# Kernel tuning notes

Measured on AMD Instinct MI355X. Metric: run time of the kernel, lower is better.

## Reference

```python
import jax, jax.numpy as jnp
import numpy as np

N_NODES = 20000
N_EDGES = 320000
F_IN = 512
F_OUT = 1024
N_GRAPHS = 64


def gcn_conv(x, src, dst, ew, W, b, n_nodes):
    xw = x @ W  # [N, Fout]
    loop = jnp.arange(n_nodes)
    s = jnp.concatenate([src, loop])
    d = jnp.concatenate([dst, loop])
    w = jnp.concatenate([ew, jnp.ones((n_nodes,), dtype=x.dtype)])
    deg = jax.ops.segment_sum(w, d, num_segments=n_nodes)  # in-degree by weight
    dinv = jnp.where(deg > 0, jax.lax.rsqrt(deg), 0.0).astype(x.dtype)
    norm = dinv[s] * w * dinv[d]  # [E+N]
    msg = norm[:, None] * xw[s]  # [E+N, Fout]
    out = jax.ops.segment_sum(msg, d, num_segments=n_nodes)
    return out + b


def mean_pool(x, batch, n_graphs):
    sums = jax.ops.segment_sum(x, batch, num_segments=n_graphs)
    cnt = jax.ops.segment_sum(jnp.ones((x.shape[0],), dtype=x.dtype), batch, num_segments=n_graphs)
    return sums / jnp.maximum(cnt, 1.0)[:, None]


def setup_inputs() -> dict:
    key = jax.random.key(0)
    ks = jax.random.split(key, 8)
    node_features = jax.random.normal(ks[0], (N_NODES, F_IN), dtype=jnp.float32)
    edge_index = jax.random.randint(ks[1], (2, N_EDGES), 0, N_NODES, dtype=jnp.int64)
    edge_weight = jax.random.uniform(ks[2], (N_EDGES,), dtype=jnp.float32)
    batch = jnp.sort(jax.random.randint(ks[3], (N_NODES,), 0, N_GRAPHS, dtype=jnp.int64))
    # Glorot-style params for the two GCNConv layers
    W1 = jax.random.normal(ks[4], (F_IN, F_OUT), dtype=jnp.float32) / np.sqrt(F_IN)
    b1 = jnp.zeros((F_OUT,), dtype=jnp.float32)
    W2 = jax.random.normal(ks[5], (F_OUT, F_OUT), dtype=jnp.float32) / np.sqrt(F_OUT)
    b2 = jnp.zeros((F_OUT,), dtype=jnp.float32)
    return {"node_features": node_features, "edge_index": edge_index,
            "edge_weight": edge_weight, "batch": batch,
            "W1": W1, "b1": b1, "W2": W2, "b2": b2}


def reference(node_features, edge_index, edge_weight, batch, W1, b1, W2, b2):
    n_nodes = node_features.shape[0]
    src, dst = edge_index[0], edge_index[1]
    h = jax.nn.relu(gcn_conv(node_features, src, dst, edge_weight, W1, b1, n_nodes))
    h = jax.nn.relu(gcn_conv(h, src, dst, edge_weight, W2, b2, n_nodes))
    return mean_pool(h, batch, N_GRAPHS)  # [G, F_OUT]
```

## Files before the change

### kernel.cpp

```cpp
#include <hip/hip_runtime.h>

#define N_NODES 20000
#define N_PAD   20480
#define N_EDGES 320000
#define F_IN 512
#define F_OUT 1024
#define N_GRAPHS 64
#define ESTRIDE 64

typedef __attribute__((ext_vector_type(8))) short bf16x8;
typedef __attribute__((ext_vector_type(4))) float f32x4;
typedef __attribute__((ext_vector_type(8))) unsigned short ushort8v;

static __device__ __forceinline__ unsigned short f2bf(float f) {
    unsigned int u = __float_as_uint(f);
    u = (u + 0x7fff + ((u >> 16) & 1)) >> 16;
    return (unsigned short)u;
}
static __device__ __forceinline__ float bf2f(unsigned short s) {
    return __uint_as_float(((unsigned int)s) << 16);
}

__global__ void k_setup(float* deg, int* cursor, float* out,
                        const int* __restrict__ batch, int* gstart,
                        unsigned int* __restrict__ csre) {
    int i = blockIdx.x * 256 + threadIdx.x;
    if (i < N_NODES) { deg[i] = 1.0f; cursor[i] = 0; }
    if (i < N_GRAPHS * F_OUT) out[i] = 0.f;
    if (i <= N_GRAPHS) {
        if (i == N_GRAPHS) gstart[i] = N_NODES;
        else {
            int lo = 0, hi = N_NODES;
            while (lo < hi) {
                int mid = (lo + hi) >> 1;
                if (batch[mid] < i) lo = mid + 1; else hi = mid;
            }
            gstart[i] = lo;
        }
    }
    for (int t = i; t < N_NODES * ESTRIDE; t += 65536) csre[t] = 0u;
}

#define NB_E    ((N_EDGES + 255) / 256)
#define NB_WT   ((F_OUT / 32) * (F_IN / 32 + F_OUT / 32))
#define NB_CX   (N_PAD * (F_IN / 8) / 256)
__global__ __launch_bounds__(256) void k_pre(const int* __restrict__ dst,
                                             const float* __restrict__ ew,
                                             float* deg,
                                             const float* __restrict__ W1,
                                             unsigned short* __restrict__ Wt1,
                                             const float* __restrict__ W2,
                                             unsigned short* __restrict__ Wt2,
                                             const float* __restrict__ x,
                                             unsigned short* __restrict__ xb) {
    __shared__ float tile[32][33];
    const int bid = blockIdx.x;
    if (bid < NB_E) {
        int e = bid * 256 + threadIdx.x;
        if (e < N_EDGES) atomicAdd(&deg[dst[e]], ew[e]);
    } else if (bid < NB_E + NB_WT) {
        int cid = bid - NB_E;
        int by = cid >> 5;
        int n0 = (cid & 31) * 32;
        const float* W; unsigned short* Wt; int K, k0;
        if (by < F_IN / 32) { W = W1; Wt = Wt1; K = F_IN;  k0 = by * 32; }
        else                { W = W2; Wt = Wt2; K = F_OUT; k0 = (by - F_IN / 32) * 32; }
        int tx = threadIdx.x & 31;
        int ty = threadIdx.x >> 5;
#pragma unroll
        for (int i = 0; i < 32; i += 8)
            tile[ty + i][tx] = W[(size_t)(k0 + ty + i) * F_OUT + n0 + tx];
        __syncthreads();
#pragma unroll
        for (int i = 0; i < 32; i += 8)
            Wt[(size_t)(n0 + ty + i) * K + k0 + tx] = f2bf(tile[tx][ty + i]);
    } else {
        int idx = (bid - NB_E - NB_WT) * 256 + threadIdx.x;
        int row = idx >> 6;
        int c8 = (idx & 63) * 8;
        if (row >= N_PAD) return;
        ushort8v v;
        if (row < N_NODES) {
            const float* p = &x[(size_t)row * F_IN + c8];
#pragma unroll
            for (int i = 0; i < 8; i++) v[i] = f2bf(p[i]);
        } else {
#pragma unroll
            for (int i = 0; i < 8; i++) v[i] = 0;
        }
        *(ushort8v*)&xb[(size_t)row * F_IN + c8] = v;
    }
}

__global__ void k_fill(const int* __restrict__ src, const int* __restrict__ dst,
                       const float* __restrict__ ew, const float* __restrict__ deg,
                       int* cursor, unsigned int* __restrict__ csre) {
    int e = blockIdx.x * 256 + threadIdx.x;
    if (e < N_EDGES) {
        int d = dst[e], s = src[e];
        int pos = atomicAdd(&cursor[d], 1);
        if (pos < ESTRIDE) {
            float w = rsqrtf(deg[s]) * ew[e] * rsqrtf(deg[d]);
            csre[d * ESTRIDE + pos] = ((unsigned int)f2bf(w) << 16) | (unsigned int)s;
        }
    }
}

__global__ __launch_bounds__(256) void k_aggr_slab(const unsigned short* __restrict__ xin,
                                                   const float* __restrict__ deg,
                                                   const int* __restrict__ cursor,
                                                   const unsigned int* __restrict__ csre,
                                                   const float* __restrict__ bias,
                                                   unsigned short* __restrict__ outp,
                                                   int F, int act) {
    const int bid = blockIdx.x;
    const int slab = bid & 7;
    const int ng = (bid >> 3) * 4 + (threadIdx.x >> 6);
    const int lane = threadIdx.x & 63;
    const int n = ng * 8 + (lane >> 3);
    const int c = blockIdx.y * 512 + slab * 64 + (lane & 7) * 8;

    if (n >= N_NODES) {
        ushort8v z;
#pragma unroll
        for (int i = 0; i < 8; i++) z[i] = 0;
        *(ushort8v*)&outp[(size_t)n * F + c] = z;
        return;
    }

    const float di = rsqrtf(deg[n]);
    const float wself = di * di;
    float a[8];
    {
        ushort8v v = *(const ushort8v*)&xin[(size_t)n * F + c];
#pragma unroll
        for (int i = 0; i < 8; i++) a[i] = bf2f(v[i]) * wself;
    }

    const unsigned int* ce = csre + (size_t)n * ESTRIDE;
    const int cnt = min(cursor[n], ESTRIDE);
    const int cnt4 = (cnt + 3) & ~3;

    if (cnt4 > 0) {
        uint4 m0 = *(const uint4*)&ce[0];
        uint4 m1 = (4 < cnt4) ? *(const uint4*)&ce[4] : m0;
        ushort8v u0 = *(const ushort8v*)&xin[(size_t)(m0.x & 0xFFFF) * F + c];
        ushort8v u1 = *(const ushort8v*)&xin[(size_t)(m0.y & 0xFFFF) * F + c];
        ushort8v u2 = *(const ushort8v*)&xin[(size_t)(m0.z & 0xFFFF) * F + c];
        ushort8v u3 = *(const ushort8v*)&xin[(size_t)(m0.w & 0xFFFF) * F + c];

        for (int j = 4; j < cnt4; j += 4) {
            ushort8v v0 = *(const ushort8v*)&xin[(size_t)(m1.x & 0xFFFF) * F + c];
            ushort8v v1 = *(const ushort8v*)&xin[(size_t)(m1.y & 0xFFFF) * F + c];
            ushort8v v2 = *(const ushort8v*)&xin[(size_t)(m1.z & 0xFFFF) * F + c];
            ushort8v v3 = *(const ushort8v*)&xin[(size_t)(m1.w & 0xFFFF) * F + c];
            const int jn = (j + 4 < cnt4) ? j + 4 : 0;
            uint4 m2 = *(const uint4*)&ce[jn];
            {
                float w0 = bf2f((unsigned short)(m0.x >> 16));
                float w1 = bf2f((unsigned short)(m0.y >> 16));
                float w2 = bf2f((unsigned short)(m0.z >> 16));
                float w3 = bf2f((unsigned short)(m0.w >> 16));
#pragma unroll
                for (int i = 0; i < 8; i++) {
                    a[i] += w0 * bf2f(u0[i]);
                    a[i] += w1 * bf2f(u1[i]);
                    a[i] += w2 * bf2f(u2[i]);
                    a[i] += w3 * bf2f(u3[i]);
                }
            }
            m0 = m1; m1 = m2;
            u0 = v0; u1 = v1; u2 = v2; u3 = v3;
        }
        {
            float w0 = bf2f((unsigned short)(m0.x >> 16));
            float w1 = bf2f((unsigned short)(m0.y >> 16));
            float w2 = bf2f((unsigned short)(m0.z >> 16));
            float w3 = bf2f((unsigned short)(m0.w >> 16));
#pragma unroll
            for (int i = 0; i < 8; i++) {
                a[i] += w0 * bf2f(u0[i]);
                a[i] += w1 * bf2f(u1[i]);
                a[i] += w2 * bf2f(u2[i]);
                a[i] += w3 * bf2f(u3[i]);
            }
        }
    }

    ushort8v r;
    if (act) {
#pragma unroll
        for (int i = 0; i < 8; i++) r[i] = f2bf(fmaxf(a[i] + bias[c + i], 0.f));
    } else {
#pragma unroll
        for (int i = 0; i < 8; i++) r[i] = f2bf(a[i]);
    }
    *(ushort8v*)&outp[(size_t)n * F + c] = r;
}

__global__ __launch_bounds__(256, 3) void k_gemm_sb(const unsigned short* __restrict__ A,
                                                    const unsigned short* __restrict__ Bt,
                                                    unsigned short* __restrict__ C, int K,
                                                    const float* __restrict__ bias, int act) {
    __shared__ short As[128 * 64];
    __shared__ short Bs[128 * 64];
    const int bid = blockIdx.x;
    const int xcd = bid & 7;
    const int i2 = bid >> 3;
    const int colb = i2 & 7;
    const int rowb = xcd * 20 + (i2 >> 3);
    const int row0 = rowb * 128;
    const int col0 = colb * 128;

    const int tid = threadIdx.x;
    const int lane = tid & 63;
    const int wave = tid >> 6;
    const int wm = wave >> 1, wn = wave & 1;
    const int l16 = lane & 15;
    const int kq = lane >> 4;

    const int NT = K >> 6;
    f32x4 acc[4][4] = {};

    for (int t = 0; t < NT; ++t) {
        const int k0 = t * 64;
#pragma unroll
        for (int it = 0; it < 4; it++) {
            int q = it * 256 + tid;
            int r = q >> 3;
            int g = (q & 7) ^ (r & 7);
            __builtin_amdgcn_global_load_lds(
                (const __attribute__((address_space(1))) void*)&A[(size_t)(row0 + r) * K + k0 + g * 8],
                (__attribute__((address_space(3))) void*)&As[q * 8], 16, 0, 0);
            __builtin_amdgcn_global_load_lds(
                (const __attribute__((address_space(1))) void*)&Bt[(size_t)(col0 + r) * K + k0 + g * 8],
                (__attribute__((address_space(3))) void*)&Bs[q * 8], 16, 0, 0);
        }
        __syncthreads();

#pragma unroll
        for (int ks = 0; ks < 2; ks++) {
            bf16x8 af[4], bfr[4];
#pragma unroll
            for (int fr = 0; fr < 4; fr++) {
                int r = wm * 64 + fr * 16 + l16;
                int g = (ks * 4 + kq) ^ (r & 7);
                af[fr] = *(const bf16x8*)&As[(r * 8 + g) * 8];
            }
#pragma unroll
            for (int fc = 0; fc < 4; fc++) {
                int r = wn * 64 + fc * 16 + l16;
                int g = (ks * 4 + kq) ^ (r & 7);
                bfr[fc] = *(const bf16x8*)&Bs[(r * 8 + g) * 8];
            }
            __builtin_amdgcn_s_setprio(1);
#pragma unroll
            for (int fr = 0; fr < 4; fr++)
#pragma unroll
                for (int fc = 0; fc < 4; fc++)
                    acc[fr][fc] = __builtin_amdgcn_mfma_f32_16x16x32_bf16(
                        af[fr], bfr[fc], acc[fr][fc], 0, 0, 0);
            __builtin_amdgcn_s_setprio(0);
        }
        __syncthreads();
    }

#pragma unroll
    for (int fr = 0; fr < 4; fr++) {
        int m0 = row0 + wm * 64 + fr * 16 + kq * 4;
#pragma unroll
        for (int fc = 0; fc < 4; fc++) {
            int n = col0 + wn * 64 + fc * 16 + l16;
            float bv = act ? bias[n] : 0.f;
#pragma unroll
            for (int reg = 0; reg < 4; reg++) {
                float v = acc[fr][fc][reg];
                if (act) v = fmaxf(v + bv, 0.f);
                C[(size_t)(m0 + reg) * F_OUT + n] = f2bf(v);
            }
        }
    }
}

__global__ __launch_bounds__(64) void k_pool_g(const unsigned short* __restrict__ h,
                                               const int* __restrict__ gstart,
                                               float* __restrict__ out) {
    const int g = blockIdx.x >> 4;
    const int slab = blockIdx.x & 15;
    const int lane = threadIdx.x;
    const int c = slab * 64 + (lane & 7) * 8;
    const int r0 = gstart[g], r1 = gstart[g + 1];

    float a[8] = {};
    for (int r = r0 + (lane >> 3); r < r1; r += 8) {
        ushort8v v = *(const ushort8v*)&h[(size_t)r * F_OUT + c];
#pragma unroll
        for (int i = 0; i < 8; i++) a[i] += bf2f(v[i]);
    }
#pragma unroll
    for (int m = 8; m < 64; m <<= 1)
#pragma unroll
        for (int i = 0; i < 8; i++) a[i] += __shfl_xor(a[i], m, 64);

    if ((lane >> 3) == 0) {
        const float inv = 1.0f / (float)max(r1 - r0, 1);
#pragma unroll
        for (int i = 0; i < 8; i++)
            out[(size_t)g * F_OUT + c + i] = a[i] * inv;
    }
}

extern "C" void kernel_launch(void* const* d_in, const int* in_sizes, int n_in,
                              void* d_out, int out_size, void* d_ws, size_t ws_size,
                              hipStream_t stream) {
    const float* x    = (const float*)d_in[0];
    const int* ei     = (const int*)d_in[1];
    const float* ew   = (const float*)d_in[2];
    const int* batch  = (const int*)d_in[3];
    const float* W1   = (const float*)d_in[4];
    const float* b1   = (const float*)d_in[5];
    const float* W2   = (const float*)d_in[6];
    const float* b2   = (const float*)d_in[7];
    float* out = (float*)d_out;

    const int* src = ei;
    const int* dst = ei + N_EDGES;

    char* ws = (char*)d_ws;
    const size_t SZ_XB  = (size_t)N_PAD * F_IN * 2;
    const size_t SZ_AX  = (size_t)N_PAD * F_IN * 2;
    const size_t SZ_WT1 = (size_t)F_OUT * F_IN * 2;
    const size_t SZ_WT2 = (size_t)F_OUT * F_OUT * 2;
    const size_t SZ_B   = (size_t)N_PAD * F_OUT * 2;
    unsigned short* xb  = (unsigned short*)(ws);
    unsigned short* ax  = (unsigned short*)(ws + SZ_XB);
    unsigned short* Wt1 = (unsigned short*)(ws + SZ_XB + SZ_AX);
    unsigned short* Wt2 = (unsigned short*)(ws + SZ_XB + SZ_AX + SZ_WT1);
    unsigned short* h1  = (unsigned short*)(ws + SZ_XB + SZ_AX + SZ_WT1 + SZ_WT2);
    unsigned short* xw2 = (unsigned short*)(ws + SZ_XB + SZ_AX + SZ_WT1 + SZ_WT2 + SZ_B);
    unsigned short* h2  = (unsigned short*)(ws);
    size_t off = SZ_XB + SZ_AX + SZ_WT1 + SZ_WT2 + 2 * SZ_B;
    auto alloc = [&](size_t bytes) -> void* {
        void* p = ws + off;
        off += (bytes + 255) & ~(size_t)255;
        return p;
    };
    float*        deg    = (float*)       alloc((size_t)N_NODES * 4);
    int*          cursor = (int*)         alloc((size_t)N_NODES * 4);
    unsigned int* csre   = (unsigned int*)alloc((size_t)N_NODES * ESTRIDE * 4);
    int*          gstart = (int*)         alloc((size_t)(N_GRAPHS + 1) * 4);

    k_setup<<<(N_GRAPHS * F_OUT + 255) / 256, 256, 0, stream>>>(deg, cursor, out, batch, gstart, csre);
    k_pre<<<NB_E + NB_WT + NB_CX, 256, 0, stream>>>(dst, ew, deg, W1, Wt1, W2, Wt2, x, xb);
    k_fill<<<NB_E, 256, 0, stream>>>(src, dst, ew, deg, cursor, csre);
    k_aggr_slab<<<dim3((N_PAD / 32) * 8, 1), 256, 0, stream>>>(xb, deg, cursor, csre,
                                                               (const float*)nullptr, ax, F_IN, 0);
    const int gemm_blocks = (N_PAD / 128) * (F_OUT / 128);
    k_gemm_sb<<<gemm_blocks, 256, 0, stream>>>(ax, Wt1, h1, F_IN, b1, 1);
    k_gemm_sb<<<gemm_blocks, 256, 0, stream>>>(h1, Wt2, xw2, F_OUT, (const float*)nullptr, 0);
    k_aggr_slab<<<dim3((N_PAD / 32) * 8, 2), 256, 0, stream>>>(xw2, deg, cursor, csre, b2, h2, F_OUT, 1);
    k_pool_g<<<N_GRAPHS * 16, 64, 0, stream>>>(h2, gstart, out);
}
```

Baseline: 313.6 us.

## Widen GEMM tile to 128x256 with 8 waves and cheapen gather address math

The GEMM kernel now uses 512-thread blocks computing 128x256 output tiles (8 waves in a 2x4 layout), halving the number of blocks and reusing each A tile across twice as many columns. In the aggregation kernel, gather addresses are computed with 32-bit shifts instead of 64-bit multiplies, and bf16 edge weights are extracted with a mask instead of shift-and-convert. The larger tile raises LDS use and register pressure per block, which may lower occupancy.

```diff
diff --git a/kernel.cpp b/kernel.cpp
--- a/kernel.cpp
+++ b/kernel.cpp
@@ -128,11 +128,15 @@
         return;
     }
 
+    const char* xb_ = (const char*)xin;
+    const unsigned shB = (F == 512) ? 10u : 11u;
+    const unsigned c2 = (unsigned)(c * 2);
+
     const float di = rsqrtf(deg[n]);
     const float wself = di * di;
     float a[8];
     {
-        ushort8v v = *(const ushort8v*)&xin[(size_t)n * F + c];
+        ushort8v v = *(const ushort8v*)(xb_ + (((unsigned)n << shB) + c2));
 #pragma unroll
         for (int i = 0; i < 8; i++) a[i] = bf2f(v[i]) * wself;
     }
@@ -144,23 +148,23 @@
     if (cnt4 > 0) {
         uint4 m0 = *(const uint4*)&ce[0];
         uint4 m1 = (4 < cnt4) ? *(const uint4*)&ce[4] : m0;
-        ushort8v u0 = *(const ushort8v*)&xin[(size_t)(m0.x & 0xFFFF) * F + c];
-        ushort8v u1 = *(const ushort8v*)&xin[(size_t)(m0.y & 0xFFFF) * F + c];
-        ushort8v u2 = *(const ushort8v*)&xin[(size_t)(m0.z & 0xFFFF) * F + c];
-        ushort8v u3 = *(const ushort8v*)&xin[(size_t)(m0.w & 0xFFFF) * F + c];
+        ushort8v u0 = *(const ushort8v*)(xb_ + (((m0.x & 0xFFFFu) << shB) + c2));
+        ushort8v u1 = *(const ushort8v*)(xb_ + (((m0.y & 0xFFFFu) << shB) + c2));
+        ushort8v u2 = *(const ushort8v*)(xb_ + (((m0.z & 0xFFFFu) << shB) + c2));
+        ushort8v u3 = *(const ushort8v*)(xb_ + (((m0.w & 0xFFFFu) << shB) + c2));
 
         for (int j = 4; j < cnt4; j += 4) {
-            ushort8v v0 = *(const ushort8v*)&xin[(size_t)(m1.x & 0xFFFF) * F + c];
-            ushort8v v1 = *(const ushort8v*)&xin[(size_t)(m1.y & 0xFFFF) * F + c];
-            ushort8v v2 = *(const ushort8v*)&xin[(size_t)(m1.z & 0xFFFF) * F + c];
-            ushort8v v3 = *(const ushort8v*)&xin[(size_t)(m1.w & 0xFFFF) * F + c];
+            ushort8v v0 = *(const ushort8v*)(xb_ + (((m1.x & 0xFFFFu) << shB) + c2));
+            ushort8v v1 = *(const ushort8v*)(xb_ + (((m1.y & 0xFFFFu) << shB) + c2));
+            ushort8v v2 = *(const ushort8v*)(xb_ + (((m1.z & 0xFFFFu) << shB) + c2));
+            ushort8v v3 = *(const ushort8v*)(xb_ + (((m1.w & 0xFFFFu) << shB) + c2));
             const int jn = (j + 4 < cnt4) ? j + 4 : 0;
             uint4 m2 = *(const uint4*)&ce[jn];
             {
-                float w0 = bf2f((unsigned short)(m0.x >> 16));
-                float w1 = bf2f((unsigned short)(m0.y >> 16));
-                float w2 = bf2f((unsigned short)(m0.z >> 16));
-                float w3 = bf2f((unsigned short)(m0.w >> 16));
+                float w0 = __uint_as_float(m0.x & 0xFFFF0000u);
+                float w1 = __uint_as_float(m0.y & 0xFFFF0000u);
+                float w2 = __uint_as_float(m0.z & 0xFFFF0000u);
+                float w3 = __uint_as_float(m0.w & 0xFFFF0000u);
 #pragma unroll
                 for (int i = 0; i < 8; i++) {
                     a[i] += w0 * bf2f(u0[i]);
@@ -173,10 +177,10 @@
             u0 = v0; u1 = v1; u2 = v2; u3 = v3;
         }
         {
-            float w0 = bf2f((unsigned short)(m0.x >> 16));
-            float w1 = bf2f((unsigned short)(m0.y >> 16));
-            float w2 = bf2f((unsigned short)(m0.z >> 16));
-            float w3 = bf2f((unsigned short)(m0.w >> 16));
+            float w0 = __uint_as_float(m0.x & 0xFFFF0000u);
+            float w1 = __uint_as_float(m0.y & 0xFFFF0000u);
+            float w2 = __uint_as_float(m0.z & 0xFFFF0000u);
+            float w3 = __uint_as_float(m0.w & 0xFFFF0000u);
 #pragma unroll
             for (int i = 0; i < 8; i++) {
                 a[i] += w0 * bf2f(u0[i]);
@@ -198,24 +202,25 @@
     *(ushort8v*)&outp[(size_t)n * F + c] = r;
 }
 
-__global__ __launch_bounds__(256, 3) void k_gemm_sb(const unsigned short* __restrict__ A,
+__global__ __launch_bounds__(512, 2) void k_gemm_sb(const unsigned short* __restrict__ A,
                                                     const unsigned short* __restrict__ Bt,
                                                     unsigned short* __restrict__ C, int K,
                                                     const float* __restrict__ bias, int act) {
     __shared__ short As[128 * 64];
-    __shared__ short Bs[128 * 64];
+    __shared__ short Bs[256 * 64];
     const int bid = blockIdx.x;
     const int xcd = bid & 7;
     const int i2 = bid >> 3;
-    const int colb = i2 & 7;
-    const int rowb = xcd * 20 + (i2 >> 3);
+    const int colb = i2 & 3;
+    const int rowb = xcd * 20 + (i2 >> 2);
     const int row0 = rowb * 128;
-    const int col0 = colb * 128;
+    const int col0 = colb * 256;
 
     const int tid = threadIdx.x;
     const int lane = tid & 63;
     const int wave = tid >> 6;
-    const int wm = wave >> 1, wn = wave & 1;
+    const int wm = wave >> 2;
+    const int wn = wave & 3;
     const int l16 = lane & 15;
     const int kq = lane >> 4;
 
@@ -225,13 +230,19 @@
     for (int t = 0; t < NT; ++t) {
         const int k0 = t * 64;
 #pragma unroll
-        for (int it = 0; it < 4; it++) {
-            int q = it * 256 + tid;
+        for (int it = 0; it < 2; it++) {
+            int q = it * 512 + tid;
             int r = q >> 3;
             int g = (q & 7) ^ (r & 7);
             __builtin_amdgcn_global_load_lds(
                 (const __attribute__((address_space(1))) void*)&A[(size_t)(row0 + r) * K + k0 + g * 8],
                 (__attribute__((address_space(3))) void*)&As[q * 8], 16, 0, 0);
+        }
+#pragma unroll
+        for (int it = 0; it < 4; it++) {
+            int q = it * 512 + tid;
+            int r = q >> 3;
+            int g = (q & 7) ^ (r & 7);
             __builtin_amdgcn_global_load_lds(
                 (const __attribute__((address_space(1))) void*)&Bt[(size_t)(col0 + r) * K + k0 + g * 8],
                 (__attribute__((address_space(3))) void*)&Bs[q * 8], 16, 0, 0);
@@ -355,9 +366,9 @@
     k_fill<<<NB_E, 256, 0, stream>>>(src, dst, ew, deg, cursor, csre);
     k_aggr_slab<<<dim3((N_PAD / 32) * 8, 1), 256, 0, stream>>>(xb, deg, cursor, csre,
                                                                (const float*)nullptr, ax, F_IN, 0);
-    const int gemm_blocks = (N_PAD / 128) * (F_OUT / 128);
-    k_gemm_sb<<<gemm_blocks, 256, 0, stream>>>(ax, Wt1, h1, F_IN, b1, 1);
-    k_gemm_sb<<<gemm_blocks, 256, 0, stream>>>(h1, Wt2, xw2, F_OUT, (const float*)nullptr, 0);
+    const int gemm_blocks = (N_PAD / 128) * (F_OUT / 256);
+    k_gemm_sb<<<gemm_blocks, 512, 0, stream>>>(ax, Wt1, h1, F_IN, b1, 1);
+    k_gemm_sb<<<gemm_blocks, 512, 0, stream>>>(h1, Wt2, xw2, F_OUT, (const float*)nullptr, 0);
     k_aggr_slab<<<dim3((N_PAD / 32) * 8, 2), 256, 0, stream>>>(xw2, deg, cursor, csre, b2, h2, F_OUT, 1);
     k_pool_g<<<N_GRAPHS * 16, 64, 0, stream>>>(h2, gstart, out);
 }
```

After: 327.9 us. 4.6% more time.
